# Performance work log

Hardware: AMD Instinct MI355X
Metric: run time of the kernel (lower is better)

## Reference

```python
import jax, jax.numpy as jnp
import numpy as np

N_NODES = 100000
N_EDGES = 1600000
N_FEAT = 500
N_CLASSES = 40


def gcn_conv(x, W, b, src, dst, n):
    """PyG GCNConv: add self-loops, symmetric deg normalization, linear + bias."""
    h = x @ W                                   # [n, out]
    loop = jnp.arange(n, dtype=src.dtype)
    s = jnp.concatenate([src, loop])            # sources incl. self-loops
    d = jnp.concatenate([dst, loop])            # destinations incl. self-loops
    deg = jax.ops.segment_sum(jnp.ones_like(d, dtype=x.dtype), d, num_segments=n)
    dinv = jax.lax.rsqrt(deg)                   # deg >= 1 because of self-loops
    norm = dinv[s] * dinv[d]                    # [E+n]
    out = jax.ops.segment_sum(h[s] * norm[:, None], d, num_segments=n)
    return out + b


def glorot(key, fan_in, fan_out):
    lim = np.sqrt(6.0 / (fan_in + fan_out)).astype(np.float32)
    return jax.random.uniform(key, (fan_in, fan_out), jnp.float32, -lim, lim)


def setup_inputs() -> dict:
    key = jax.random.key(0)
    ks = jax.random.split(key, 6)
    x = jax.random.normal(ks[0], (N_NODES, N_FEAT), dtype=jnp.float32)
    edge_index = jax.random.randint(ks[1], (2, N_EDGES), 0, N_NODES, dtype=jnp.int64)
    return {
        "x": x,
        "edge_index": edge_index,
        "W1": glorot(ks[2], N_FEAT, 128), "b1": jnp.zeros((128,), jnp.float32),
        "W2": glorot(ks[3], 128, 64),     "b2": jnp.zeros((64,), jnp.float32),
        "W4": glorot(ks[4], 64, N_CLASSES), "b4": jnp.zeros((N_CLASSES,), jnp.float32),
    }


def reference(x, edge_index, W1, b1, W2, b2, W4, b4):
    src, dst = edge_index[0], edge_index[1]
    n = x.shape[0]
    h = jax.nn.relu(gcn_conv(x, W1, b1, src, dst, n))
    h = jax.nn.relu(gcn_conv(h, W2, b2, src, dst, n))
    h = gcn_conv(h, W4, b4, src, dst, n)
    return jax.nn.log_softmax(h, axis=1)
```

## Files before the change

kernel.cpp:

```cpp
#include <hip/hip_runtime.h>
#include <hip/hip_bf16.h>
#include <cmath>

#define NNODES 100000
#define NEDGES 1600000
#define SCAN_B 1024

typedef __attribute__((ext_vector_type(8))) short bf16x8;
typedef __attribute__((ext_vector_type(4))) float f32x4;

__device__ __forceinline__ unsigned short f2bf(float f) {
    unsigned u = __builtin_bit_cast(unsigned, f);
    unsigned r = (u + 0x7fffu + ((u >> 16) & 1u)) >> 16;
    return (unsigned short)r;
}
__device__ __forceinline__ float bflo(unsigned v) {
    return __builtin_bit_cast(float, v << 16);
}
__device__ __forceinline__ float bfhi(unsigned v) {
    return __builtin_bit_cast(float, v & 0xffff0000u);
}


__global__ void zero_deg(int* __restrict__ deg, int n) {
    int i = blockIdx.x * 256 + threadIdx.x;
    if (i < n) deg[i] = 0;
}

__global__ __launch_bounds__(256) void count_deg_xcd(const int* __restrict__ dst,
                                                     int* __restrict__ deg, int E) {
    int g = blockIdx.x & 7;
    int sub = blockIdx.x >> 3;
    int nsub = gridDim.x >> 3;
    int lo = g * (NNODES / 8), hi = lo + (NNODES / 8);
    for (int e = sub * 256 + threadIdx.x; e < E; e += nsub * 256) {
        int d = dst[e];
        if (d >= lo && d < hi) atomicAdd(&deg[d], 1);
    }
}

__global__ void calc_dinv(const int* __restrict__ deg, float* __restrict__ dinv, int n) {
    int i = blockIdx.x * 256 + threadIdx.x;
    if (i < n) dinv[i] = rsqrtf(1.0f + (float)deg[i]);
}

__global__ __launch_bounds__(SCAN_B) void scan_block(const int* __restrict__ deg,
                                                     int* __restrict__ pos,
                                                     int* __restrict__ bsums, int n) {
    __shared__ int s[SCAN_B];
    int tid = threadIdx.x;
    int gid = blockIdx.x * SCAN_B + tid;
    int v = (gid < n) ? deg[gid] : 0;
    s[tid] = v;
    __syncthreads();
    for (int off = 1; off < SCAN_B; off <<= 1) {
        int t = (tid >= off) ? s[tid - off] : 0;
        __syncthreads();
        s[tid] += t;
        __syncthreads();
    }
    if (gid < n) pos[gid] = s[tid] - v;
    if (tid == SCAN_B - 1) bsums[blockIdx.x] = s[tid];
}

__global__ __launch_bounds__(128) void scan_sums(int* __restrict__ bsums, int nb) {
    __shared__ int s[128];
    int tid = threadIdx.x;
    int v = (tid < nb) ? bsums[tid] : 0;
    s[tid] = v;
    __syncthreads();
    for (int off = 1; off < 128; off <<= 1) {
        int t = (tid >= off) ? s[tid - off] : 0;
        __syncthreads();
        s[tid] += t;
        __syncthreads();
    }
    if (tid < nb) bsums[tid] = s[tid] - v;
}

__global__ __launch_bounds__(SCAN_B) void add_off(int* __restrict__ pos,
                                                  const int* __restrict__ bsums, int n) {
    int gid = blockIdx.x * SCAN_B + threadIdx.x;
    if (gid < n) pos[gid] += bsums[blockIdx.x];
}

__global__ __launch_bounds__(256) void csr_fill_xcd(const int* __restrict__ src,
                                                    const int* __restrict__ dst,
                                                    int* __restrict__ pos,
                                                    int* __restrict__ csr_src, int E) {
    int g = blockIdx.x & 7;
    int sub = blockIdx.x >> 3;
    int nsub = gridDim.x >> 3;
    int lo = g * (NNODES / 8), hi = lo + (NNODES / 8);
    for (int e = sub * 256 + threadIdx.x; e < E; e += nsub * 256) {
        int d = dst[e];
        if (d >= lo && d < hi) {
            int slot = atomicAdd(&pos[d], 1);
            csr_src[slot] = src[e];
        }
    }
}


__global__ __launch_bounds__(256) void conv_w1t(const float* __restrict__ W1,
                                                unsigned short* __restrict__ W1t) {
    int t = blockIdx.x * 256 + threadIdx.x;
    if (t >= 128 * 512) return;
    int n = t >> 9, k = t & 511;
    W1t[t] = (k < 500) ? f2bf(W1[k * 128 + n]) : (unsigned short)0;
}

__global__ __launch_bounds__(256) void conv_w2t(const float* __restrict__ W2,
                                                unsigned short* __restrict__ W2t) {
    int t = blockIdx.x * 256 + threadIdx.x;
    if (t >= 64 * 128) return;
    int n = t >> 7, k = t & 127;
    W2t[t] = f2bf(W2[k * 64 + n]);
}


__global__ __launch_bounds__(256) void gemm1_mfma(
    const float* __restrict__ x, const unsigned short* __restrict__ W1t,
    const float* __restrict__ dinv, unsigned short* __restrict__ C, int M)
{
    __shared__ short sA[4096];
    __shared__ short sB[4096];
    const int tid = threadIdx.x;
    const int w = tid >> 6;
    const int l = tid & 63;
    const int lm = l & 15;
    const int q = l >> 4;
    const int row0 = blockIdx.x * 128;

    f32x4 acc[2][8];
    #pragma unroll
    for (int i = 0; i < 2; i++)
        #pragma unroll
        for (int j = 0; j < 8; j++) acc[i][j] = (f32x4){0.f, 0.f, 0.f, 0.f};

    for (int k0 = 0; k0 < 512; k0 += 32) {
        __syncthreads();
        #pragma unroll
        for (int rep = 0; rep < 2; rep++) {
            int b = tid + rep * 256;
            int qq = b >> 7, m = b & 127;
            int r = row0 + m; if (r >= M) r = M - 1;
            int kb = k0 + qq * 8;
            bf16x8 o;
            if (kb + 8 <= 500) {
                float4 u = *(const float4*)(x + (size_t)r * 500 + kb);
                float4 v = *(const float4*)(x + (size_t)r * 500 + kb + 4);
                o[0] = f2bf(u.x); o[1] = f2bf(u.y); o[2] = f2bf(u.z); o[3] = f2bf(u.w);
                o[4] = f2bf(v.x); o[5] = f2bf(v.y); o[6] = f2bf(v.z); o[7] = f2bf(v.w);
            } else {
                #pragma unroll
                for (int j = 0; j < 8; j++) {
                    int k = kb + j;
                    o[j] = (k < 500) ? (short)f2bf(x[(size_t)r * 500 + k]) : (short)0;
                }
            }
            *(bf16x8*)&sA[b * 8] = o;
        }
        #pragma unroll
        for (int rep = 0; rep < 2; rep++) {
            int b = tid + rep * 256;
            int qq = b >> 7, n = b & 127;
            bf16x8 v = *(const bf16x8*)(W1t + (size_t)n * 512 + k0 + qq * 8);
            *(bf16x8*)&sB[b * 8] = v;
        }
        __syncthreads();
        bf16x8 af[2];
        #pragma unroll
        for (int i = 0; i < 2; i++)
            af[i] = *(const bf16x8*)&sA[(q * 128 + w * 32 + i * 16 + lm) * 8];
        bf16x8 bfr[8];
        #pragma unroll
        for (int j = 0; j < 8; j++)
            bfr[j] = *(const bf16x8*)&sB[(q * 128 + j * 16 + lm) * 8];
        #pragma unroll
        for (int i = 0; i < 2; i++)
            #pragma unroll
            for (int j = 0; j < 8; j++)
                acc[i][j] = __builtin_amdgcn_mfma_f32_16x16x32_bf16(af[i], bfr[j], acc[i][j], 0, 0, 0);
    }

    #pragma unroll
    for (int i = 0; i < 2; i++) {
        #pragma unroll
        for (int reg = 0; reg < 4; reg++) {
            int grow = row0 + w * 32 + i * 16 + q * 4 + reg;
            if (grow < M) {
                float d = dinv[grow];
                #pragma unroll
                for (int j = 0; j < 8; j++)
                    C[(size_t)grow * 128 + j * 16 + lm] = f2bf(d * acc[i][j][reg]);
            }
        }
    }
}


__global__ __launch_bounds__(256) void gemm2_mfma(
    const unsigned short* __restrict__ A, const unsigned short* __restrict__ Bt,
    const float* __restrict__ dinv, unsigned short* __restrict__ C, int M)
{
    __shared__ short sA[4096];
    __shared__ short sB[2048];
    const int tid = threadIdx.x;
    const int w = tid >> 6;
    const int l = tid & 63;
    const int lm = l & 15;
    const int q = l >> 4;
    const int row0 = blockIdx.x * 128;

    f32x4 acc[2][4];
    #pragma unroll
    for (int i = 0; i < 2; i++)
        #pragma unroll
        for (int j = 0; j < 4; j++) acc[i][j] = (f32x4){0.f, 0.f, 0.f, 0.f};

    for (int k0 = 0; k0 < 128; k0 += 32) {
        __syncthreads();
        #pragma unroll
        for (int rep = 0; rep < 2; rep++) {
            int b = tid + rep * 256;
            int qq = b >> 7, m = b & 127;
            int r = row0 + m; if (r >= M) r = M - 1;
            *(bf16x8*)&sA[b * 8] = *(const bf16x8*)(A + (size_t)r * 128 + k0 + qq * 8);
        }
        {
            int b = tid;
            int qq = b >> 6, n = b & 63;
            *(bf16x8*)&sB[b * 8] = *(const bf16x8*)(Bt + (size_t)n * 128 + k0 + qq * 8);
        }
        __syncthreads();
        bf16x8 af[2];
        #pragma unroll
        for (int i = 0; i < 2; i++)
            af[i] = *(const bf16x8*)&sA[(q * 128 + w * 32 + i * 16 + lm) * 8];
        bf16x8 bfr[4];
        #pragma unroll
        for (int j = 0; j < 4; j++)
            bfr[j] = *(const bf16x8*)&sB[(q * 64 + j * 16 + lm) * 8];
        #pragma unroll
        for (int i = 0; i < 2; i++)
            #pragma unroll
            for (int j = 0; j < 4; j++)
                acc[i][j] = __builtin_amdgcn_mfma_f32_16x16x32_bf16(af[i], bfr[j], acc[i][j], 0, 0, 0);
    }

    #pragma unroll
    for (int i = 0; i < 2; i++) {
        #pragma unroll
        for (int reg = 0; reg < 4; reg++) {
            int grow = row0 + w * 32 + i * 16 + q * 4 + reg;
            if (grow < M) {
                float d = dinv[grow];
                #pragma unroll
                for (int j = 0; j < 4; j++)
                    C[(size_t)grow * 64 + j * 16 + lm] = f2bf(d * acc[i][j][reg]);
            }
        }
    }
}


__global__ __launch_bounds__(256) void gemm_n40(
    const float* __restrict__ A, const float* __restrict__ W,
    const float* __restrict__ bias, const float* __restrict__ dinv,
    float* __restrict__ C, int M)
{
    __shared__ float sA[32][65];
    __shared__ float sW[64][40];
    const int row0 = blockIdx.x * 32;
    for (int idx = threadIdx.x; idx < 64 * 40; idx += 256)
        sW[idx / 40][idx % 40] = W[idx];
    for (int idx = threadIdx.x; idx < 32 * 64; idx += 256) {
        int r = idx >> 6, k = idx & 63;
        int row = row0 + r;
        float v = 0.0f;
        if (row < M) v = fmaxf(A[(long)row * 64 + k] + bias[k], 0.0f);
        sA[r][k] = v;
    }
    __syncthreads();
    float acc[5] = {0, 0, 0, 0, 0};
    int rr[5], cc[5];
    #pragma unroll
    for (int j = 0; j < 5; j++) {
        int o = threadIdx.x + 256 * j;
        rr[j] = o / 40; cc[j] = o % 40;
    }
    for (int k = 0; k < 64; k++) {
        #pragma unroll
        for (int j = 0; j < 5; j++) acc[j] += sA[rr[j]][k] * sW[k][cc[j]];
    }
    #pragma unroll
    for (int j = 0; j < 5; j++) {
        int row = row0 + rr[j];
        if (row < M) C[(long)row * 40 + cc[j]] = dinv[row] * acc[j];
    }
}


template<int F, bool OBF16>
__global__ __launch_bounds__(256) void gather_bf(
    const unsigned short* __restrict__ h, const float* __restrict__ dinv,
    const int* __restrict__ pos, const int* __restrict__ csr_src,
    void* __restrict__ outv, const float* __restrict__ bias, int n)
{
    constexpr int P = F / 2;
    unsigned t = blockIdx.x * 256u + threadIdx.x;
    unsigned node = t / P;
    unsigned p = t - node * P;
    if (node >= (unsigned)n) return;
    int e0 = node ? pos[node - 1] : 0;
    int e1 = pos[node];
    float di = dinv[node];
    unsigned sv = *(const unsigned*)(h + (size_t)node * F + 2 * p);
    float a0 = bflo(sv);
    float a1 = bfhi(sv);
    int j = e0;
    for (; j + 4 <= e1; j += 4) {
        int s0 = csr_src[j], s1 = csr_src[j + 1], s2 = csr_src[j + 2], s3 = csr_src[j + 3];
        unsigned v0 = *(const unsigned*)(h + (size_t)s0 * F + 2 * p);
        unsigned v1 = *(const unsigned*)(h + (size_t)s1 * F + 2 * p);
        unsigned v2 = *(const unsigned*)(h + (size_t)s2 * F + 2 * p);
        unsigned v3 = *(const unsigned*)(h + (size_t)s3 * F + 2 * p);
        a0 += bflo(v0) + bflo(v1) + bflo(v2) + bflo(v3);
        a1 += bfhi(v0) + bfhi(v1) + bfhi(v2) + bfhi(v3);
    }
    for (; j < e1; j++) {
        int s = csr_src[j];
        unsigned v = *(const unsigned*)(h + (size_t)s * F + 2 * p);
        a0 += bflo(v);
        a1 += bfhi(v);
    }
    a0 *= di; a1 *= di;
    if constexpr (OBF16) {
        a0 = fmaxf(a0 + bias[2 * p], 0.0f);
        a1 = fmaxf(a1 + bias[2 * p + 1], 0.0f);
        ((unsigned*)outv)[(size_t)node * P + p] =
            ((unsigned)f2bf(a1) << 16) | (unsigned)f2bf(a0);
    } else {
        float2 r; r.x = a0; r.y = a1;
        ((float2*)outv)[(size_t)node * P + p] = r;
    }
}


template<int F>
__global__ __launch_bounds__(256) void gather_agg(
    const float* __restrict__ h, const float* __restrict__ dinv,
    const int* __restrict__ pos, const int* __restrict__ csr_src,
    float* __restrict__ out, int n)
{
    unsigned t = blockIdx.x * 256u + threadIdx.x;
    unsigned node = t / F;
    unsigned c = t - node * F;
    if (node >= (unsigned)n) return;
    int e0 = node ? pos[node - 1] : 0;
    int e1 = pos[node];
    float di = dinv[node];
    float acc = h[(size_t)node * F + c];
    int j = e0;
    for (; j + 4 <= e1; j += 4) {
        int s0 = csr_src[j], s1 = csr_src[j + 1], s2 = csr_src[j + 2], s3 = csr_src[j + 3];
        float v0 = h[(size_t)s0 * F + c];
        float v1 = h[(size_t)s1 * F + c];
        float v2 = h[(size_t)s2 * F + c];
        float v3 = h[(size_t)s3 * F + c];
        acc += v0 + v1 + v2 + v3;
    }
    for (; j < e1; j++) {
        int s = csr_src[j];
        acc += h[(size_t)s * F + c];
    }
    out[(size_t)node * F + c] = di * acc;
}


__global__ __launch_bounds__(256) void logsoftmax40(const float* __restrict__ h,
                                                    const float* __restrict__ bias,
                                                    float* __restrict__ out, int n) {
    int wave = (blockIdx.x * 256 + threadIdx.x) >> 6;
    int lane = threadIdx.x & 63;
    if (wave >= n) return;
    float x = 0.0f, v = -INFINITY;
    if (lane < 40) { x = h[(long)wave * 40 + lane] + bias[lane]; v = x; }
    #pragma unroll
    for (int off = 32; off; off >>= 1) v = fmaxf(v, __shfl_xor(v, off, 64));
    float ex = (lane < 40) ? expf(x - v) : 0.0f;
    float s = ex;
    #pragma unroll
    for (int off = 32; off; off >>= 1) s += __shfl_xor(s, off, 64);
    if (lane < 40) out[(long)wave * 40 + lane] = x - v - logf(s);
}


extern "C" void kernel_launch(void* const* d_in, const int* in_sizes, int n_in,
                              void* d_out, int out_size, void* d_ws, size_t ws_size,
                              hipStream_t stream) {
    const float* x  = (const float*)d_in[0];
    const int*   ei = (const int*)d_in[1];
    const float* W1 = (const float*)d_in[2];
    const float* b1 = (const float*)d_in[3];
    const float* W2 = (const float*)d_in[4];
    const float* b2 = (const float*)d_in[5];
    const float* W4 = (const float*)d_in[6];
    const float* b4 = (const float*)d_in[7];
    float* out = (float*)d_out;
    float* ws  = (float*)d_ws;

    const int N = NNODES, E = NEDGES;
    const int* src = ei;
    const int* dst = ei + E;

    float*          dinv    = ws;
    int*            deg     = (int*)(ws + 100000);
    int*            pos     = (int*)(ws + 200000);
    int*            bsums   = (int*)(ws + 300000);
    int*            csr_src = (int*)(ws + 300200);
    unsigned short* W1t     = (unsigned short*)(ws + 1900200);
    unsigned short* W2t     = (unsigned short*)(ws + 1933000);
    unsigned short* h1      = (unsigned short*)(ws + 1937100);
    unsigned short* h2      = (unsigned short*)(ws + 1937100);
    unsigned short* a1      = (unsigned short*)(ws + 8337100);
    float*          h3      = ws + 8337100;
    float*          a2      = ws + 14737100;
    float*          a3      = out;

    const int nscan = (N + SCAN_B - 1) / SCAN_B;

    zero_deg<<<(N + 255) / 256, 256, 0, stream>>>(deg, N);
    count_deg_xcd<<<1024, 256, 0, stream>>>(dst, deg, E);
    calc_dinv<<<(N + 255) / 256, 256, 0, stream>>>(deg, dinv, N);
    scan_block<<<nscan, SCAN_B, 0, stream>>>(deg, pos, bsums, N);
    scan_sums<<<1, 128, 0, stream>>>(bsums, nscan);
    add_off<<<nscan, SCAN_B, 0, stream>>>(pos, bsums, N);
    csr_fill_xcd<<<1024, 256, 0, stream>>>(src, dst, pos, csr_src, E);

    conv_w1t<<<(128 * 512 + 255) / 256, 256, 0, stream>>>(W1, W1t);
    conv_w2t<<<(64 * 128 + 255) / 256, 256, 0, stream>>>(W2, W2t);

    gemm1_mfma<<<(N + 127) / 128, 256, 0, stream>>>(x, W1t, dinv, h1, N);
    {
        unsigned tot = (unsigned)N * 64u;
        gather_bf<128, true><<<(tot + 255) / 256, 256, 0, stream>>>(h1, dinv, pos, csr_src, a1, b1, N);
    }

    gemm2_mfma<<<(N + 127) / 128, 256, 0, stream>>>(a1, W2t, dinv, h2, N);
    {
        unsigned tot = (unsigned)N * 32u;
        gather_bf<64, false><<<(tot + 255) / 256, 256, 0, stream>>>(h2, dinv, pos, csr_src, a2, nullptr, N);
    }

    gemm_n40<<<(N + 31) / 32, 256, 0, stream>>>(a2, W4, b2, dinv, h3, N);
    {
        unsigned tot = (unsigned)N * 40u;
        gather_agg<40><<<(tot + 255) / 256, 256, 0, stream>>>(h3, dinv, pos, csr_src, a3, N);
    }

    logsoftmax40<<<(N * 64 + 255) / 256, 256, 0, stream>>>(a3, b4, out, N);
}
```

Baseline: 772.3 us.

## Double-buffer LDS tiles in gemm1 to overlap global loads with MFMA

The first-layer GEMM kernel now keeps two LDS buffers for the A and B tiles and prefetches the next k-slice from global memory into registers while MFMAs run on the current slice. Each iteration then converts and stores the prefetched slice into the other buffer. This removes one barrier per iteration and hides global load latency. In exchange it doubles shared memory use and raises register pressure, which may lower occupancy. The boundary handling for the 500-wide feature dimension is also simplified to float4 granularity.

```diff
diff --git a/kernel.cpp b/kernel.cpp
--- a/kernel.cpp
+++ b/kernel.cpp
@@ -123,8 +123,8 @@
     const float* __restrict__ x, const unsigned short* __restrict__ W1t,
     const float* __restrict__ dinv, unsigned short* __restrict__ C, int M)
 {
-    __shared__ short sA[4096];
-    __shared__ short sB[4096];
+    __shared__ short sA[2][4096];
+    __shared__ short sB[2][4096];
     const int tid = threadIdx.x;
     const int w = tid >> 6;
     const int l = tid & 63;
@@ -138,50 +138,88 @@
         #pragma unroll
         for (int j = 0; j < 8; j++) acc[i][j] = (f32x4){0.f, 0.f, 0.f, 0.f};
 
-    for (int k0 = 0; k0 < 512; k0 += 32) {
-        __syncthreads();
-        #pragma unroll
-        for (int rep = 0; rep < 2; rep++) {
-            int b = tid + rep * 256;
-            int qq = b >> 7, m = b & 127;
-            int r = row0 + m; if (r >= M) r = M - 1;
-            int kb = k0 + qq * 8;
-            bf16x8 o;
-            if (kb + 8 <= 500) {
-                float4 u = *(const float4*)(x + (size_t)r * 500 + kb);
-                float4 v = *(const float4*)(x + (size_t)r * 500 + kb + 4);
-                o[0] = f2bf(u.x); o[1] = f2bf(u.y); o[2] = f2bf(u.z); o[3] = f2bf(u.w);
-                o[4] = f2bf(v.x); o[5] = f2bf(v.y); o[6] = f2bf(v.z); o[7] = f2bf(v.w);
-            } else {
-                #pragma unroll
-                for (int j = 0; j < 8; j++) {
-                    int k = kb + j;
-                    o[j] = (k < 500) ? (short)f2bf(x[(size_t)r * 500 + k]) : (short)0;
-                }
+    int akq[2];
+    const float* aptr[2];
+    const unsigned short* bptr[2];
+    #pragma unroll
+    for (int rep = 0; rep < 2; rep++) {
+        int b = tid + rep * 256;
+        akq[rep] = (b >> 7) * 8;
+        int m = b & 127;
+        int r = row0 + m; if (r >= M) r = M - 1;
+        aptr[rep] = x + (size_t)r * 500;
+        bptr[rep] = W1t + (size_t)(b & 127) * 512;
+    }
+
+    const float4 z4 = {0.f, 0.f, 0.f, 0.f};
+    float4 u[2], v[2];
+    bf16x8 bb[2];
+
+    #pragma unroll
+    for (int rep = 0; rep < 2; rep++) {
+        int kb = akq[rep];
+        u[rep] = *(const float4*)(aptr[rep] + kb);
+        v[rep] = *(const float4*)(aptr[rep] + kb + 4);
+        bb[rep] = *(const bf16x8*)(bptr[rep] + akq[rep]);
+    }
+    #pragma unroll
+    for (int rep = 0; rep < 2; rep++) {
+        int b = tid + rep * 256;
+        bf16x8 o;
+        o[0] = f2bf(u[rep].x); o[1] = f2bf(u[rep].y);
+        o[2] = f2bf(u[rep].z); o[3] = f2bf(u[rep].w);
+        o[4] = f2bf(v[rep].x); o[5] = f2bf(v[rep].y);
+        o[6] = f2bf(v[rep].z); o[7] = f2bf(v[rep].w);
+        *(bf16x8*)&sA[0][b * 8] = o;
+        *(bf16x8*)&sB[0][b * 8] = bb[rep];
+    }
+    __syncthreads();
+
+    for (int it = 0; it < 16; ++it) {
+        const int cur = it & 1;
+        const int nxt = cur ^ 1;
+        const bool more = (it + 1 < 16);
+
+        if (more) {
+            int k0 = (it + 1) * 32;
+            #pragma unroll
+            for (int rep = 0; rep < 2; rep++) {
+                int kb = k0 + akq[rep];
+                u[rep] = (kb + 4 <= 500) ? *(const float4*)(aptr[rep] + kb)     : z4;
+                v[rep] = (kb + 8 <= 500) ? *(const float4*)(aptr[rep] + kb + 4) : z4;
+                bb[rep] = *(const bf16x8*)(bptr[rep] + kb);
             }
-            *(bf16x8*)&sA[b * 8] = o;
-        }
-        #pragma unroll
-        for (int rep = 0; rep < 2; rep++) {
-            int b = tid + rep * 256;
-            int qq = b >> 7, n = b & 127;
-            bf16x8 v = *(const bf16x8*)(W1t + (size_t)n * 512 + k0 + qq * 8);
-            *(bf16x8*)&sB[b * 8] = v;
-        }
-        __syncthreads();
-        bf16x8 af[2];
-        #pragma unroll
-        for (int i = 0; i < 2; i++)
-            af[i] = *(const bf16x8*)&sA[(q * 128 + w * 32 + i * 16 + lm) * 8];
-        bf16x8 bfr[8];
-        #pragma unroll
-        for (int j = 0; j < 8; j++)
-            bfr[j] = *(const bf16x8*)&sB[(q * 128 + j * 16 + lm) * 8];
-        #pragma unroll
-        for (int i = 0; i < 2; i++)
+        }
+
+        {
+            bf16x8 af[2], bfr[8];
+            #pragma unroll
+            for (int i = 0; i < 2; i++)
+                af[i] = *(const bf16x8*)&sA[cur][(q * 128 + w * 32 + i * 16 + lm) * 8];
             #pragma unroll
             for (int j = 0; j < 8; j++)
-                acc[i][j] = __builtin_amdgcn_mfma_f32_16x16x32_bf16(af[i], bfr[j], acc[i][j], 0, 0, 0);
+                bfr[j] = *(const bf16x8*)&sB[cur][(q * 128 + j * 16 + lm) * 8];
+            #pragma unroll
+            for (int i = 0; i < 2; i++)
+                #pragma unroll
+                for (int j = 0; j < 8; j++)
+                    acc[i][j] = __builtin_amdgcn_mfma_f32_16x16x32_bf16(af[i], bfr[j], acc[i][j], 0, 0, 0);
+        }
+
+        if (more) {
+            #pragma unroll
+            for (int rep = 0; rep < 2; rep++) {
+                int b = tid + rep * 256;
+                bf16x8 o;
+                o[0] = f2bf(u[rep].x); o[1] = f2bf(u[rep].y);
+                o[2] = f2bf(u[rep].z); o[3] = f2bf(u[rep].w);
+                o[4] = f2bf(v[rep].x); o[5] = f2bf(v[rep].y);
+                o[6] = f2bf(v[rep].z); o[7] = f2bf(v[rep].w);
+                *(bf16x8*)&sA[nxt][b * 8] = o;
+                *(bf16x8*)&sB[nxt][b * 8] = bb[rep];
+            }
+            __syncthreads();
+        }
     }
 
     #pragma unroll
```

New measurement: 835.1 us. 8.1% more time.

## Pre-swizzle weights into MFMA fragment layout and drop LDS staging in GEMMs

Applied to the files above, without the earlier changes.

Weight conversion kernels now write W1 and W2 directly in the per-lane MFMA fragment order, so each lane loads its B fragment with one contiguous 16-byte global load. The two GEMMs no longer stage A and B through shared memory with barriers; each lane reads its own A rows straight from global memory and converts to bf16 in registers. This removes LDS traffic and __syncthreads, at the cost of redundant global and L2 reads of B across waves and less coalesced A loads, since each lane reads 32 bytes from a different row.

```diff
diff --git a/kernel.cpp b/kernel.cpp
--- a/kernel.cpp
+++ b/kernel.cpp
@@ -102,29 +102,47 @@
 }
 
 
-__global__ __launch_bounds__(256) void conv_w1t(const float* __restrict__ W1,
-                                                unsigned short* __restrict__ W1t) {
-    int t = blockIdx.x * 256 + threadIdx.x;
-    if (t >= 128 * 512) return;
-    int n = t >> 9, k = t & 511;
-    W1t[t] = (k < 500) ? f2bf(W1[k * 128 + n]) : (unsigned short)0;
-}
-
-__global__ __launch_bounds__(256) void conv_w2t(const float* __restrict__ W2,
-                                                unsigned short* __restrict__ W2t) {
-    int t = blockIdx.x * 256 + threadIdx.x;
-    if (t >= 64 * 128) return;
-    int n = t >> 7, k = t & 127;
-    W2t[t] = f2bf(W2[k * 64 + n]);
+__global__ __launch_bounds__(256) void conv_w1f(const float* __restrict__ W1,
+                                                unsigned short* __restrict__ W1f) {
+    int idx = blockIdx.x * 256 + threadIdx.x;
+    if (idx >= 8192) return;
+    int t = idx >> 9;
+    int rest = idx & 511;
+    int j = rest >> 6;
+    int l = rest & 63;
+    int n = j * 16 + (l & 15);
+    int kb = t * 32 + (l >> 4) * 8;
+    bf16x8 o;
+    #pragma unroll
+    for (int jj = 0; jj < 8; jj++) {
+        int k = kb + jj;
+        o[jj] = (k < 500) ? (short)f2bf(W1[k * 128 + n]) : (short)0;
+    }
+    *(bf16x8*)(W1f + (size_t)idx * 8) = o;
+}
+
+__global__ __launch_bounds__(256) void conv_w2f(const float* __restrict__ W2,
+                                                unsigned short* __restrict__ W2f) {
+    int idx = blockIdx.x * 256 + threadIdx.x;
+    if (idx >= 1024) return;
+    int t = idx >> 8;
+    int rest = idx & 255;
+    int j = rest >> 6;
+    int l = rest & 63;
+    int n = j * 16 + (l & 15);
+    int kb = t * 32 + (l >> 4) * 8;
+    bf16x8 o;
+    #pragma unroll
+    for (int jj = 0; jj < 8; jj++)
+        o[jj] = (short)f2bf(W2[(kb + jj) * 64 + n]);
+    *(bf16x8*)(W2f + (size_t)idx * 8) = o;
 }
 
 
 __global__ __launch_bounds__(256) void gemm1_mfma(
-    const float* __restrict__ x, const unsigned short* __restrict__ W1t,
+    const float* __restrict__ x, const unsigned short* __restrict__ W1f,
     const float* __restrict__ dinv, unsigned short* __restrict__ C, int M)
 {
-    __shared__ short sA[4096];
-    __shared__ short sB[4096];
     const int tid = threadIdx.x;
     const int w = tid >> 6;
     const int l = tid & 63;
@@ -132,51 +150,49 @@
     const int q = l >> 4;
     const int row0 = blockIdx.x * 128;
 
+    const float* abase[2];
+    #pragma unroll
+    for (int i = 0; i < 2; i++) {
+        int r = row0 + w * 32 + i * 16 + lm;
+        if (r >= M) r = M - 1;
+        abase[i] = x + (size_t)r * 500 + q * 8;
+    }
+
     f32x4 acc[2][8];
     #pragma unroll
     for (int i = 0; i < 2; i++)
         #pragma unroll
         for (int j = 0; j < 8; j++) acc[i][j] = (f32x4){0.f, 0.f, 0.f, 0.f};
 
-    for (int k0 = 0; k0 < 512; k0 += 32) {
-        __syncthreads();
-        #pragma unroll
-        for (int rep = 0; rep < 2; rep++) {
-            int b = tid + rep * 256;
-            int qq = b >> 7, m = b & 127;
-            int r = row0 + m; if (r >= M) r = M - 1;
-            int kb = k0 + qq * 8;
-            bf16x8 o;
-            if (kb + 8 <= 500) {
-                float4 u = *(const float4*)(x + (size_t)r * 500 + kb);
-                float4 v = *(const float4*)(x + (size_t)r * 500 + kb + 4);
+    for (int t = 0; t < 16; ++t) {
+        const int k0 = t * 32;
+        bf16x8 af[2];
+        if (k0 + q * 8 + 8 <= 500) {
+            #pragma unroll
+            for (int i = 0; i < 2; i++) {
+                float4 u = *(const float4*)(abase[i] + k0);
+                float4 v = *(const float4*)(abase[i] + k0 + 4);
+                bf16x8 o;
                 o[0] = f2bf(u.x); o[1] = f2bf(u.y); o[2] = f2bf(u.z); o[3] = f2bf(u.w);
                 o[4] = f2bf(v.x); o[5] = f2bf(v.y); o[6] = f2bf(v.z); o[7] = f2bf(v.w);
-            } else {
+                af[i] = o;
+            }
+        } else {
+            #pragma unroll
+            for (int i = 0; i < 2; i++) {
+                bf16x8 o;
                 #pragma unroll
-                for (int j = 0; j < 8; j++) {
-                    int k = kb + j;
-                    o[j] = (k < 500) ? (short)f2bf(x[(size_t)r * 500 + k]) : (short)0;
+                for (int jj = 0; jj < 8; jj++) {
+                    int k = k0 + q * 8 + jj;
+                    o[jj] = (k < 500) ? (short)f2bf(abase[i][k0 + jj]) : (short)0;
                 }
+                af[i] = o;
             }
-            *(bf16x8*)&sA[b * 8] = o;
         }
-        #pragma unroll
-        for (int rep = 0; rep < 2; rep++) {
-            int b = tid + rep * 256;
-            int qq = b >> 7, n = b & 127;
-            bf16x8 v = *(const bf16x8*)(W1t + (size_t)n * 512 + k0 + qq * 8);
-            *(bf16x8*)&sB[b * 8] = v;
-        }
-        __syncthreads();
-        bf16x8 af[2];
-        #pragma unroll
-        for (int i = 0; i < 2; i++)
-            af[i] = *(const bf16x8*)&sA[(q * 128 + w * 32 + i * 16 + lm) * 8];
         bf16x8 bfr[8];
         #pragma unroll
         for (int j = 0; j < 8; j++)
-            bfr[j] = *(const bf16x8*)&sB[(q * 128 + j * 16 + lm) * 8];
+            bfr[j] = *(const bf16x8*)(W1f + (((size_t)t * 8 + j) * 64 + l) * 8);
         #pragma unroll
         for (int i = 0; i < 2; i++)
             #pragma unroll
@@ -201,11 +217,9 @@
 
 
 __global__ __launch_bounds__(256) void gemm2_mfma(
-    const unsigned short* __restrict__ A, const unsigned short* __restrict__ Bt,
+    const unsigned short* __restrict__ A, const unsigned short* __restrict__ W2f,
     const float* __restrict__ dinv, unsigned short* __restrict__ C, int M)
 {
-    __shared__ short sA[4096];
-    __shared__ short sB[2048];
     const int tid = threadIdx.x;
     const int w = tid >> 6;
     const int l = tid & 63;
@@ -213,35 +227,30 @@
     const int q = l >> 4;
     const int row0 = blockIdx.x * 128;
 
+    const unsigned short* abase[2];
+    #pragma unroll
+    for (int i = 0; i < 2; i++) {
+        int r = row0 + w * 32 + i * 16 + lm;
+        if (r >= M) r = M - 1;
+        abase[i] = A + (size_t)r * 128 + q * 8;
+    }
+
     f32x4 acc[2][4];
     #pragma unroll
     for (int i = 0; i < 2; i++)
         #pragma unroll
         for (int j = 0; j < 4; j++) acc[i][j] = (f32x4){0.f, 0.f, 0.f, 0.f};
 
-    for (int k0 = 0; k0 < 128; k0 += 32) {
-        __syncthreads();
-        #pragma unroll
-        for (int rep = 0; rep < 2; rep++) {
-            int b = tid + rep * 256;
-            int qq = b >> 7, m = b & 127;
-            int r = row0 + m; if (r >= M) r = M - 1;
-            *(bf16x8*)&sA[b * 8] = *(const bf16x8*)(A + (size_t)r * 128 + k0 + qq * 8);
-        }
-        {
-            int b = tid;
-            int qq = b >> 6, n = b & 63;
-            *(bf16x8*)&sB[b * 8] = *(const bf16x8*)(Bt + (size_t)n * 128 + k0 + qq * 8);
-        }
-        __syncthreads();
+    for (int t = 0; t < 4; ++t) {
+        const int k0 = t * 32;
         bf16x8 af[2];
         #pragma unroll
         for (int i = 0; i < 2; i++)
-            af[i] = *(const bf16x8*)&sA[(q * 128 + w * 32 + i * 16 + lm) * 8];
+            af[i] = *(const bf16x8*)(abase[i] + k0);
         bf16x8 bfr[4];
         #pragma unroll
         for (int j = 0; j < 4; j++)
-            bfr[j] = *(const bf16x8*)&sB[(q * 64 + j * 16 + lm) * 8];
+            bfr[j] = *(const bf16x8*)(W2f + (((size_t)t * 4 + j) * 64 + l) * 8);
         #pragma unroll
         for (int i = 0; i < 2; i++)
             #pragma unroll
@@ -420,8 +429,8 @@
     int*            pos     = (int*)(ws + 200000);
     int*            bsums   = (int*)(ws + 300000);
     int*            csr_src = (int*)(ws + 300200);
-    unsigned short* W1t     = (unsigned short*)(ws + 1900200);
-    unsigned short* W2t     = (unsigned short*)(ws + 1933000);
+    unsigned short* W1f     = (unsigned short*)(ws + 1900200);
+    unsigned short* W2f     = (unsigned short*)(ws + 1933000);
     unsigned short* h1      = (unsigned short*)(ws + 1937100);
     unsigned short* h2      = (unsigned short*)(ws + 1937100);
     unsigned short* a1      = (unsigned short*)(ws + 8337100);
@@ -439,16 +448,16 @@
     add_off<<<nscan, SCAN_B, 0, stream>>>(pos, bsums, N);
     csr_fill_xcd<<<1024, 256, 0, stream>>>(src, dst, pos, csr_src, E);
 
-    conv_w1t<<<(128 * 512 + 255) / 256, 256, 0, stream>>>(W1, W1t);
-    conv_w2t<<<(64 * 128 + 255) / 256, 256, 0, stream>>>(W2, W2t);
-
-    gemm1_mfma<<<(N + 127) / 128, 256, 0, stream>>>(x, W1t, dinv, h1, N);
+    conv_w1f<<<32, 256, 0, stream>>>(W1, W1f);
+    conv_w2f<<<4, 256, 0, stream>>>(W2, W2f);
+
+    gemm1_mfma<<<(N + 127) / 128, 256, 0, stream>>>(x, W1f, dinv, h1, N);
     {
         unsigned tot = (unsigned)N * 64u;
         gather_bf<128, true><<<(tot + 255) / 256, 256, 0, stream>>>(h1, dinv, pos, csr_src, a1, b1, N);
     }
 
-    gemm2_mfma<<<(N + 127) / 128, 256, 0, stream>>>(a1, W2t, dinv, h2, N);
+    gemm2_mfma<<<(N + 127) / 128, 256, 0, stream>>>(a1, W2f, dinv, h2, N);
     {
         unsigned tot = (unsigned)N * 32u;
         gather_bf<64, false><<<(tot + 255) / 256, 256, 0, stream>>>(h2, dinv, pos, csr_src, a2, nullptr, N);
```

Result: no change. 764.3 us (-1.0%).
